# Optimization experiments

Measured on AMD Instinct MI355X. Metric: run time of the kernel, lower is better.

The kernel has to match this reference:

```python
import jax, jax.numpy as jnp
import numpy as np


def _conv(x, w):
    # NCHW 'same' conv, stride 1 (kernel 7 -> pad 3 each side)
    return jax.lax.conv_general_dilated(
        x, w, window_strides=(1, 1), padding='SAME',
        dimension_numbers=('NCHW', 'OIHW', 'NCHW'))


def _run_dir(x, w_ih, w_hh, b, reverse):
    # x: (B, T, C, H, W); returns (B, T, hid, H, W)
    B, T, C, H, W = x.shape
    hid = w_hh.shape[1]
    # Precompute input-to-gate convs for all timesteps at once (fold T into batch)
    xg = _conv(x.reshape(B * T, C, H, W), w_ih) + b[None, :, None, None]
    xg = xg.reshape(B, T, 4 * hid, H, W).transpose(1, 0, 2, 3, 4)  # (T,B,4hid,H,W)
    h0 = jnp.zeros((B, hid, H, W), x.dtype)
    c0 = jnp.zeros_like(h0)

    def step(carry, g_x):
        h, c = carry
        g = g_x + _conv(h, w_hh)
        i, f, gg, o = jnp.split(g, 4, axis=1)  # PyTorch LSTM gate order
        c = jax.nn.sigmoid(f) * c + jax.nn.sigmoid(i) * jnp.tanh(gg)
        h = jax.nn.sigmoid(o) * jnp.tanh(c)
        return (h, c), h

    _, hs = jax.lax.scan(step, (h0, c0), xg, reverse=reverse)
    return hs.transpose(1, 0, 2, 3, 4)  # (B,T,hid,H,W)


def setup_inputs() -> dict:
    key = jax.random.key(0)
    ks = jax.random.split(key, 6)
    B, T, C, H, W = 8, 16, 3, 32, 32
    hid, K = 64, 7
    s_ih = 1.0 / np.sqrt(C * K * K)
    s_hh = 1.0 / np.sqrt(hid * K * K)
    return {
        'x': jax.random.normal(ks[0], (B, T, C, H, W), jnp.float32),
        'w_ih_f': jax.random.normal(ks[1], (4 * hid, C, K, K), jnp.float32) * s_ih,
        'w_hh_f': jax.random.normal(ks[2], (4 * hid, hid, K, K), jnp.float32) * s_hh,
        'b_f': jnp.zeros((4 * hid,), jnp.float32),
        'w_ih_b': jax.random.normal(ks[3], (4 * hid, C, K, K), jnp.float32) * s_ih,
        'w_hh_b': jax.random.normal(ks[4], (4 * hid, hid, K, K), jnp.float32) * s_hh,
        'b_b': jnp.zeros((4 * hid,), jnp.float32),
    }


def reference(x, w_ih_f, w_hh_f, b_f, w_ih_b, w_hh_b, b_b):
    out_f = _run_dir(x, w_ih_f, w_hh_f, b_f, reverse=False)
    out_b = _run_dir(x, w_ih_b, w_hh_b, b_b, reverse=True)
    # bidirectional concat along channel dim -> (B, T, 2*hid, H, W)
    return jnp.concatenate([out_f, out_b], axis=2)
```

## Files before the change

kernel.cpp:

```cpp
#include <hip/hip_runtime.h>
#include <hip/hip_bf16.h>


#define HP0_B  0
#define HP1_B  3112960
#define C_B    6225920
#define WALL_B 10420224
#define BIAS_B 13860864
#define FLAG_B 13862912

using short8 = __attribute__((ext_vector_type(8))) short;
using f32x4  = __attribute__((ext_vector_type(4))) float;

__device__ __forceinline__ float sigm(float x) { return 1.0f / (1.0f + __expf(-x)); }
__device__ __forceinline__ float tanh_f(float x) {
    x = fminf(fmaxf(x, -30.0f), 30.0f);
    float e = __expf(2.0f * x);
    return (e - 1.0f) / (e + 1.0f);
}

__global__ void detect_dtype(const unsigned int* __restrict__ xw, int* __restrict__ flag) {
    int lane = threadIdx.x;
    int cnt = 0;
    for (int i = 0; i < 4; ++i) {
        unsigned int w = xw[lane * 4 + i];
        unsigned int e = (w >> 7) & 0xFFu;
        cnt += (e >= 0xC0u) ? 1 : 0;
    }
#pragma unroll
    for (int off = 32; off > 0; off >>= 1) cnt += __shfl_down(cnt, off, 64);
    if (lane == 0) *flag = (cnt > 16) ? 1 : 0;
}

__global__ void prep_weights(const void* __restrict__ whhf, const void* __restrict__ whhb,
                             const void* __restrict__ wihf, const void* __restrict__ wihb,
                             const void* __restrict__ bf, const void* __restrict__ bb,
                             short* __restrict__ wall, float* __restrict__ bias_r,
                             const int* __restrict__ flag) {
    int n = blockIdx.x * blockDim.x + threadIdx.x;
    const int fp32 = *flag;
    if (n < 1720320) {
        int icl = n & 31;
        int oc = (n >> 5) & 255;
        int ks = (n >> 13) % 105;
        int d = n / 860160;
        const void* hh = d ? whhb : whhf;
        const void* ih = d ? wihb : wihf;
        float v = 0.0f;
        if (ks < 98) {
            int ky = ks / 14, rr = ks % 14, kc = rr / 7, kx = rr % 7;
            int si = ((oc * 64 + kc * 32 + icl) * 7 + ky) * 7 + kx;
            v = fp32 ? ((const float*)hh)[si] : __bfloat162float(((const __hip_bfloat16*)hh)[si]);
        } else {
            int kx = ks - 98, ky = icl >> 2, ic = icl & 3;
            if (ic < 3 && ky < 7) {
                int si = ((oc * 3 + ic) * 7 + ky) * 7 + kx;
                v = fp32 ? ((const float*)ih)[si] : __bfloat162float(((const __hip_bfloat16*)ih)[si]);
            }
        }
        __hip_bfloat16 hv = __float2bfloat16(v);
        wall[n] = *(short*)&hv;
        return;
    }
    n -= 1720320;
    if (n < 512) {
        const void* src = (n >= 256) ? bb : bf;
        int j = n & 255;
        bias_r[n] = fp32 ? ((const float*)src)[j] : __bfloat162float(((const __hip_bfloat16*)src)[j]);
    }
}

__global__ void zero_state(float* __restrict__ ws_f) {
    int n = blockIdx.x * blockDim.x + threadIdx.x;
    if (n < 2605056) ws_f[n] = 0.0f;
}

__global__ __launch_bounds__(512, 2)
void lstm_step(const void* __restrict__ xin,
               const short* __restrict__ wall,
               const float* __restrict__ bias_r,
               const unsigned short* __restrict__ hp_r,
               unsigned short* __restrict__ hp_w,
               float* __restrict__ c,
               void* __restrict__ out,
               const int* __restrict__ flag, int s) {
    const int ygrp = blockIdx.x;
    const int b = blockIdx.y;
    const int dir = blockIdx.z;
    const int t = dir ? (15 - s) : s;
    const int y0 = ygrp * 2;
    const int tid = threadIdx.x;
    const int wv = tid >> 6;
    const int kg = wv >> 2;
    const int wm = wv & 3;
    const int l = tid & 63;
    const int q = l >> 4;
    const int li = l & 15;
    const int fp32 = *flag;
    const int db = dir * 8 + b;

    __shared__ __align__(16) short lds[26240];

    {
        const uint4* src = (const uint4*)(hp_r + (size_t)(db * 38 + y0) * 40 * 64);
        for (int i = tid; i < 2560; i += 512) {
            int ic8 = i & 7, col = (i >> 3) % 40, row = i / 320;
            uint4 v = src[i];
            *(uint4*)&lds[(row * 40 + col) * 72 + ic8 * 8] = v;
        }
    }
    for (int i = tid; i < 3200; i += 512) {
        int k = i % 40, cc = (i / 40) % 40, r = i / 1600;
        float v = 0.0f;
        if (k < 28) {
            int ky = k >> 2, ic = k & 3;
            int yin = y0 + r + ky - 3, cin = cc - 3;
            if (ic < 3 && yin >= 0 && yin < 32 && cin >= 0 && cin < 32) {
                size_t gi = (size_t)((b * 16 + t) * 3 + ic) * 1024 + yin * 32 + cin;
                v = fp32 ? ((const float*)xin)[gi]
                         : __bfloat162float(((const __hip_bfloat16*)xin)[gi]);
            }
        }
        __hip_bfloat16 hb = __float2bfloat16(v);
        lds[23040 + i] = *(short*)&hb;
    }
    __syncthreads();

    f32x4 acc[4][4];
    if (kg == 0) {
        const float* bp = bias_r + dir * 256 + wm * 16 + q * 4;
#pragma unroll
        for (int g = 0; g < 4; ++g) {
            f32x4 bv = *(const f32x4*)(bp + g * 64);
#pragma unroll
            for (int nt = 0; nt < 4; ++nt) acc[g][nt] = bv;
        }
    } else {
        f32x4 z = {0.0f, 0.0f, 0.0f, 0.0f};
#pragma unroll
        for (int g = 0; g < 4; ++g)
#pragma unroll
            for (int nt = 0; nt < 4; ++nt) acc[g][nt] = z;
    }

    const short* wbase = wall + (size_t)dir * 860160 + ((wm * 16 + li) * 32 + q * 8);
    int bh[4], bx[4];
#pragma unroll
    for (int nt = 0; nt < 4; ++nt) {
        int rt = nt >> 1, ct = nt & 1;
        bh[nt] = (rt * 40 + ct * 16 + li) * 72 + q * 8;
        bx[nt] = 23040 + (rt * 40 + ct * 16 + li) * 40 + q * 8;
    }

    auto loadA = [&](short8* A, int ks) {
        const short* p = wbase + (size_t)ks * 8192;
#pragma unroll
        for (int g = 0; g < 4; ++g) A[g] = *(const short8*)(p + g * 2048);
    };
    auto loadB = [&](short8* B, int ks) {
        if (ks < 98) {
            int ky = ks / 14, rr = ks % 14;
            int uoff = ky * 2880 + (rr % 7) * 72 + (rr / 7) * 32;
#pragma unroll
            for (int nt = 0; nt < 4; ++nt) B[nt] = *(const short8*)&lds[bh[nt] + uoff];
        } else {
            int uoff = (ks - 98) * 40;
#pragma unroll
            for (int nt = 0; nt < 4; ++nt) B[nt] = *(const short8*)&lds[bx[nt] + uoff];
        }
    };
    auto mfma16 = [&](short8* A, short8* B) {
#pragma unroll
        for (int g = 0; g < 4; ++g)
#pragma unroll
            for (int nt = 0; nt < 4; ++nt)
                acc[g][nt] = __builtin_amdgcn_mfma_f32_16x16x32_bf16(A[g], B[nt], acc[g][nt], 0, 0, 0);
    };

    const int ks_begin = kg ? 52 : 0;
    const int ks_end   = kg ? 105 : 52;
    short8 A0[4], A1[4], B0[4], B1[4];
    loadA(A0, ks_begin); loadB(B0, ks_begin);
    int ks = ks_begin;
#pragma unroll 1
    for (; ks + 1 < ks_end; ks += 2) {
        loadA(A1, ks + 1); loadB(B1, ks + 1);
        mfma16(A0, B0);
        int kn = (ks + 2 < ks_end) ? ks + 2 : ks;
        loadA(A0, kn); loadB(B0, kn);
        mfma16(A1, B1);
    }
    if (ks < ks_end) mfma16(A0, B0);

    __syncthreads();
    {
        float* exch = (float*)lds;
        float* xp = exch + wm * 2048 + q * 64 + li * 4;
        if (kg == 1) {
#pragma unroll
            for (int g = 0; g < 2; ++g)
#pragma unroll
                for (int nt = 0; nt < 4; ++nt)
                    *(f32x4*)(xp + (g * 4 + nt) * 256) = acc[g][nt];
        }
        __syncthreads();
        if (kg == 0) {
#pragma unroll
            for (int g = 0; g < 2; ++g)
#pragma unroll
                for (int nt = 0; nt < 4; ++nt)
                    acc[g][nt] += *(const f32x4*)(xp + (g * 4 + nt) * 256);
        }
        __syncthreads();
        if (kg == 1) {
#pragma unroll
            for (int g = 0; g < 2; ++g)
#pragma unroll
                for (int nt = 0; nt < 4; ++nt)
                    *(f32x4*)(xp + (g * 4 + nt) * 256) = acc[2 + g][nt];
        }
        __syncthreads();
        if (kg == 0) {
#pragma unroll
            for (int g = 0; g < 2; ++g)
#pragma unroll
                for (int nt = 0; nt < 4; ++nt)
                    acc[2 + g][nt] += *(const f32x4*)(xp + (g * 4 + nt) * 256);
        }
    }
    if (kg == 1) return;

    const int hid0 = wm * 16 + q * 4;
#pragma unroll
    for (int nt = 0; nt < 4; ++nt) {
        int y = y0 + (nt >> 1);
        int px = (nt & 1) * 16 + li;
        float* cp = c + (size_t)(db * 1024 + y * 32 + px) * 64 + hid0;
        f32x4 cold = *(const f32x4*)cp;
        f32x4 hv;
#pragma unroll
        for (int r = 0; r < 4; ++r) {
            float iv = sigm(acc[0][nt][r]);
            float fv = sigm(acc[1][nt][r]);
            float gv = tanh_f(acc[2][nt][r]);
            float ov = sigm(acc[3][nt][r]);
            float cn = fv * cold[r] + iv * gv;
            cold[r] = cn;
            hv[r] = ov * tanh_f(cn);
        }
        *(f32x4*)cp = cold;

        ushort4 hu;
        {
            __hip_bfloat16 t0 = __float2bfloat16(hv[0]); hu.x = *(unsigned short*)&t0;
            __hip_bfloat16 t1 = __float2bfloat16(hv[1]); hu.y = *(unsigned short*)&t1;
            __hip_bfloat16 t2 = __float2bfloat16(hv[2]); hu.z = *(unsigned short*)&t2;
            __hip_bfloat16 t3 = __float2bfloat16(hv[3]); hu.w = *(unsigned short*)&t3;
        }
        *(ushort4*)(hp_w + (size_t)((db * 38 + y + 3) * 40 + px + 3) * 64 + hid0) = hu;

        size_t ob = (size_t)((b * 16 + t) * 128 + dir * 64 + hid0) * 1024 + y * 32 + px;
        if (fp32) {
            float* op = (float*)out;
#pragma unroll
            for (int r = 0; r < 4; ++r) op[ob + (size_t)r * 1024] = hv[r];
        } else {
            __hip_bfloat16* op = (__hip_bfloat16*)out;
#pragma unroll
            for (int r = 0; r < 4; ++r) op[ob + (size_t)r * 1024] = __float2bfloat16(hv[r]);
        }
    }
}

extern "C" void kernel_launch(void* const* d_in, const int* in_sizes, int n_in,
                              void* d_out, int out_size, void* d_ws, size_t ws_size,
                              hipStream_t stream) {
    char* wsb = (char*)d_ws;
    unsigned short* hp0 = (unsigned short*)(wsb + HP0_B);
    unsigned short* hp1 = (unsigned short*)(wsb + HP1_B);
    float* c = (float*)(wsb + C_B);
    short* wall = (short*)(wsb + WALL_B);
    float* bias_r = (float*)(wsb + BIAS_B);
    int* flag = (int*)(wsb + FLAG_B);

    detect_dtype<<<1, 64, 0, stream>>>((const unsigned int*)d_in[0], flag);
    prep_weights<<<6722, 256, 0, stream>>>(d_in[2], d_in[5], d_in[1], d_in[4],
                                           d_in[3], d_in[6], wall, bias_r, flag);
    zero_state<<<10176, 256, 0, stream>>>((float*)d_ws);

    for (int s = 0; s < 16; ++s) {
        unsigned short* hr = (s & 1) ? hp1 : hp0;
        unsigned short* hw = (s & 1) ? hp0 : hp1;
        lstm_step<<<dim3(16, 8, 2), 512, 0, stream>>>(d_in[0], wall, bias_r,
                                                      hr, hw, c, d_out, flag, s);
    }
}
```

Before: 645.8 us.

## Fuse timestep launches into persistent kernel with per-sequence global barriers

Replaces the 16 per-timestep kernel launches with a single persistent kernel of 256 blocks that loops over timesteps internally. The 16 blocks working on each (direction, batch) sequence synchronize through an atomic-counter spin barrier in global memory between steps, so launch overhead and the device-wide launch boundary go away. MFMA sections also get raised wave priority via s_setprio. The design relies on all 256 blocks being co-resident (2 blocks/CU), and the spin barrier has a guard timeout that could silently break ordering if it fires.

```diff
diff --git a/kernel.cpp b/kernel.cpp
--- a/kernel.cpp
+++ b/kernel.cpp
@@ -8,6 +8,7 @@
 #define WALL_B 10420224
 #define BIAS_B 13860864
 #define FLAG_B 13862912
+#define CNT_B  13862916
 
 using short8 = __attribute__((ext_vector_type(8))) short;
 using f32x4  = __attribute__((ext_vector_type(4))) float;
@@ -75,19 +76,34 @@
     if (n < 2605056) ws_f[n] = 0.0f;
 }
 
+__device__ __forceinline__ void db_barrier(int* cnt, int target) {
+    if (threadIdx.x == 0) {
+        __threadfence();
+        __hip_atomic_fetch_add(cnt, 1, __ATOMIC_RELEASE, __HIP_MEMORY_SCOPE_AGENT);
+        int guard = 0;
+        while (__hip_atomic_load(cnt, __ATOMIC_ACQUIRE, __HIP_MEMORY_SCOPE_AGENT) < target) {
+            __builtin_amdgcn_s_sleep(2);
+            if (++guard > (1 << 24)) break;
+        }
+        __threadfence();
+    }
+    __syncthreads();
+}
+
 __global__ __launch_bounds__(512, 2)
-void lstm_step(const void* __restrict__ xin,
-               const short* __restrict__ wall,
-               const float* __restrict__ bias_r,
-               const unsigned short* __restrict__ hp_r,
-               unsigned short* __restrict__ hp_w,
-               float* __restrict__ c,
-               void* __restrict__ out,
-               const int* __restrict__ flag, int s) {
-    const int ygrp = blockIdx.x;
-    const int b = blockIdx.y;
-    const int dir = blockIdx.z;
-    const int t = dir ? (15 - s) : s;
+void lstm_run(const void* __restrict__ xin,
+              const short* __restrict__ wall,
+              const float* __restrict__ bias_r,
+              unsigned short* __restrict__ hp0,
+              unsigned short* __restrict__ hp1,
+              float* __restrict__ c,
+              void* __restrict__ out,
+              const int* __restrict__ flag,
+              int s0, int s1, int* __restrict__ cnt) {
+    const int bid = blockIdx.x;
+    const int dir = bid & 1;
+    const int b = (bid >> 1) & 7;
+    const int ygrp = bid >> 4;
     const int y0 = ygrp * 2;
     const int tid = threadIdx.x;
     const int wv = tid >> 6;
@@ -101,48 +117,6 @@
 
     __shared__ __align__(16) short lds[26240];
 
-    {
-        const uint4* src = (const uint4*)(hp_r + (size_t)(db * 38 + y0) * 40 * 64);
-        for (int i = tid; i < 2560; i += 512) {
-            int ic8 = i & 7, col = (i >> 3) % 40, row = i / 320;
-            uint4 v = src[i];
-            *(uint4*)&lds[(row * 40 + col) * 72 + ic8 * 8] = v;
-        }
-    }
-    for (int i = tid; i < 3200; i += 512) {
-        int k = i % 40, cc = (i / 40) % 40, r = i / 1600;
-        float v = 0.0f;
-        if (k < 28) {
-            int ky = k >> 2, ic = k & 3;
-            int yin = y0 + r + ky - 3, cin = cc - 3;
-            if (ic < 3 && yin >= 0 && yin < 32 && cin >= 0 && cin < 32) {
-                size_t gi = (size_t)((b * 16 + t) * 3 + ic) * 1024 + yin * 32 + cin;
-                v = fp32 ? ((const float*)xin)[gi]
-                         : __bfloat162float(((const __hip_bfloat16*)xin)[gi]);
-            }
-        }
-        __hip_bfloat16 hb = __float2bfloat16(v);
-        lds[23040 + i] = *(short*)&hb;
-    }
-    __syncthreads();
-
-    f32x4 acc[4][4];
-    if (kg == 0) {
-        const float* bp = bias_r + dir * 256 + wm * 16 + q * 4;
-#pragma unroll
-        for (int g = 0; g < 4; ++g) {
-            f32x4 bv = *(const f32x4*)(bp + g * 64);
-#pragma unroll
-            for (int nt = 0; nt < 4; ++nt) acc[g][nt] = bv;
-        }
-    } else {
-        f32x4 z = {0.0f, 0.0f, 0.0f, 0.0f};
-#pragma unroll
-        for (int g = 0; g < 4; ++g)
-#pragma unroll
-            for (int nt = 0; nt < 4; ++nt) acc[g][nt] = z;
-    }
-
     const short* wbase = wall + (size_t)dir * 860160 + ((wm * 16 + li) * 32 + q * 8);
     int bh[4], bx[4];
 #pragma unroll
@@ -151,124 +125,179 @@
         bh[nt] = (rt * 40 + ct * 16 + li) * 72 + q * 8;
         bx[nt] = 23040 + (rt * 40 + ct * 16 + li) * 40 + q * 8;
     }
-
-    auto loadA = [&](short8* A, int ks) {
-        const short* p = wbase + (size_t)ks * 8192;
-#pragma unroll
-        for (int g = 0; g < 4; ++g) A[g] = *(const short8*)(p + g * 2048);
-    };
-    auto loadB = [&](short8* B, int ks) {
-        if (ks < 98) {
-            int ky = ks / 14, rr = ks % 14;
-            int uoff = ky * 2880 + (rr % 7) * 72 + (rr / 7) * 32;
-#pragma unroll
-            for (int nt = 0; nt < 4; ++nt) B[nt] = *(const short8*)&lds[bh[nt] + uoff];
-        } else {
-            int uoff = (ks - 98) * 40;
-#pragma unroll
-            for (int nt = 0; nt < 4; ++nt) B[nt] = *(const short8*)&lds[bx[nt] + uoff];
-        }
-    };
-    auto mfma16 = [&](short8* A, short8* B) {
-#pragma unroll
-        for (int g = 0; g < 4; ++g)
-#pragma unroll
-            for (int nt = 0; nt < 4; ++nt)
-                acc[g][nt] = __builtin_amdgcn_mfma_f32_16x16x32_bf16(A[g], B[nt], acc[g][nt], 0, 0, 0);
-    };
-
     const int ks_begin = kg ? 52 : 0;
     const int ks_end   = kg ? 105 : 52;
-    short8 A0[4], A1[4], B0[4], B1[4];
-    loadA(A0, ks_begin); loadB(B0, ks_begin);
-    int ks = ks_begin;
+
 #pragma unroll 1
-    for (; ks + 1 < ks_end; ks += 2) {
-        loadA(A1, ks + 1); loadB(B1, ks + 1);
-        mfma16(A0, B0);
-        int kn = (ks + 2 < ks_end) ? ks + 2 : ks;
-        loadA(A0, kn); loadB(B0, kn);
-        mfma16(A1, B1);
-    }
-    if (ks < ks_end) mfma16(A0, B0);
-
-    __syncthreads();
-    {
-        float* exch = (float*)lds;
-        float* xp = exch + wm * 2048 + q * 64 + li * 4;
-        if (kg == 1) {
-#pragma unroll
-            for (int g = 0; g < 2; ++g)
+    for (int s = s0; s < s1; ++s) {
+        const int t = dir ? (15 - s) : s;
+        const unsigned short* hp_r = (s & 1) ? hp1 : hp0;
+        unsigned short* hp_w = (s & 1) ? hp0 : hp1;
+
+        {
+            const uint4* src = (const uint4*)(hp_r + (size_t)(db * 38 + y0) * 40 * 64);
+            for (int i = tid; i < 2560; i += 512) {
+                int ic8 = i & 7, col = (i >> 3) % 40, row = i / 320;
+                uint4 v = src[i];
+                *(uint4*)&lds[(row * 40 + col) * 72 + ic8 * 8] = v;
+            }
+        }
+        for (int i = tid; i < 3200; i += 512) {
+            int k = i % 40, cc = (i / 40) % 40, r = i / 1600;
+            float v = 0.0f;
+            if (k < 28) {
+                int ky = k >> 2, ic = k & 3;
+                int yin = y0 + r + ky - 3, cin = cc - 3;
+                if (ic < 3 && yin >= 0 && yin < 32 && cin >= 0 && cin < 32) {
+                    size_t gi = (size_t)((b * 16 + t) * 3 + ic) * 1024 + yin * 32 + cin;
+                    v = fp32 ? ((const float*)xin)[gi]
+                             : __bfloat162float(((const __hip_bfloat16*)xin)[gi]);
+                }
+            }
+            __hip_bfloat16 hb = __float2bfloat16(v);
+            lds[23040 + i] = *(short*)&hb;
+        }
+        __syncthreads();
+
+        f32x4 acc[4][4];
+        if (kg == 0) {
+            const float* bp = bias_r + dir * 256 + wm * 16 + q * 4;
+#pragma unroll
+            for (int g = 0; g < 4; ++g) {
+                f32x4 bv = *(const f32x4*)(bp + g * 64);
+#pragma unroll
+                for (int nt = 0; nt < 4; ++nt) acc[g][nt] = bv;
+            }
+        } else {
+            f32x4 z = {0.0f, 0.0f, 0.0f, 0.0f};
+#pragma unroll
+            for (int g = 0; g < 4; ++g)
+#pragma unroll
+                for (int nt = 0; nt < 4; ++nt) acc[g][nt] = z;
+        }
+
+        auto loadA = [&](short8* A, int ks) {
+            const short* p = wbase + (size_t)ks * 8192;
+#pragma unroll
+            for (int g = 0; g < 4; ++g) A[g] = *(const short8*)(p + g * 2048);
+        };
+        auto loadB = [&](short8* B, int ks) {
+            if (ks < 98) {
+                int ky = ks / 14, rr = ks % 14;
+                int uoff = ky * 2880 + (rr % 7) * 72 + (rr / 7) * 32;
+#pragma unroll
+                for (int nt = 0; nt < 4; ++nt) B[nt] = *(const short8*)&lds[bh[nt] + uoff];
+            } else {
+                int uoff = (ks - 98) * 40;
+#pragma unroll
+                for (int nt = 0; nt < 4; ++nt) B[nt] = *(const short8*)&lds[bx[nt] + uoff];
+            }
+        };
+        auto mfma16 = [&](short8* A, short8* B) {
+            __builtin_amdgcn_s_setprio(1);
+#pragma unroll
+            for (int g = 0; g < 4; ++g)
 #pragma unroll
                 for (int nt = 0; nt < 4; ++nt)
-                    *(f32x4*)(xp + (g * 4 + nt) * 256) = acc[g][nt];
-        }
+                    acc[g][nt] = __builtin_amdgcn_mfma_f32_16x16x32_bf16(A[g], B[nt], acc[g][nt], 0, 0, 0);
+            __builtin_amdgcn_s_setprio(0);
+        };
+
+        short8 A0[4], A1[4], B0[4], B1[4];
+        loadA(A0, ks_begin); loadB(B0, ks_begin);
+        int ks = ks_begin;
+#pragma unroll 1
+        for (; ks + 1 < ks_end; ks += 2) {
+            loadA(A1, ks + 1); loadB(B1, ks + 1);
+            mfma16(A0, B0);
+            int kn = (ks + 2 < ks_end) ? ks + 2 : ks;
+            loadA(A0, kn); loadB(B0, kn);
+            mfma16(A1, B1);
+        }
+        if (ks < ks_end) mfma16(A0, B0);
+
         __syncthreads();
+        {
+            float* exch = (float*)lds;
+            float* xp = exch + wm * 2048 + q * 64 + li * 4;
+            if (kg == 1) {
+#pragma unroll
+                for (int g = 0; g < 2; ++g)
+#pragma unroll
+                    for (int nt = 0; nt < 4; ++nt)
+                        *(f32x4*)(xp + (g * 4 + nt) * 256) = acc[g][nt];
+            }
+            __syncthreads();
+            if (kg == 0) {
+#pragma unroll
+                for (int g = 0; g < 2; ++g)
+#pragma unroll
+                    for (int nt = 0; nt < 4; ++nt)
+                        acc[g][nt] += *(const f32x4*)(xp + (g * 4 + nt) * 256);
+            }
+            __syncthreads();
+            if (kg == 1) {
+#pragma unroll
+                for (int g = 0; g < 2; ++g)
+#pragma unroll
+                    for (int nt = 0; nt < 4; ++nt)
+                        *(f32x4*)(xp + (g * 4 + nt) * 256) = acc[2 + g][nt];
+            }
+            __syncthreads();
+            if (kg == 0) {
+#pragma unroll
+                for (int g = 0; g < 2; ++g)
+#pragma unroll
+                    for (int nt = 0; nt < 4; ++nt)
+                        acc[2 + g][nt] += *(const f32x4*)(xp + (g * 4 + nt) * 256);
+            }
+        }
+
         if (kg == 0) {
-#pragma unroll
-            for (int g = 0; g < 2; ++g)
-#pragma unroll
-                for (int nt = 0; nt < 4; ++nt)
-                    acc[g][nt] += *(const f32x4*)(xp + (g * 4 + nt) * 256);
-        }
+            const int hid0 = wm * 16 + q * 4;
+#pragma unroll
+            for (int nt = 0; nt < 4; ++nt) {
+                int y = y0 + (nt >> 1);
+                int px = (nt & 1) * 16 + li;
+                float* cp = c + (size_t)(db * 1024 + y * 32 + px) * 64 + hid0;
+                f32x4 cold = *(const f32x4*)cp;
+                f32x4 hv;
+#pragma unroll
+                for (int r = 0; r < 4; ++r) {
+                    float iv = sigm(acc[0][nt][r]);
+                    float fv = sigm(acc[1][nt][r]);
+                    float gv = tanh_f(acc[2][nt][r]);
+                    float ov = sigm(acc[3][nt][r]);
+                    float cn = fv * cold[r] + iv * gv;
+                    cold[r] = cn;
+                    hv[r] = ov * tanh_f(cn);
+                }
+                *(f32x4*)cp = cold;
+
+                ushort4 hu;
+                {
+                    __hip_bfloat16 t0 = __float2bfloat16(hv[0]); hu.x = *(unsigned short*)&t0;
+                    __hip_bfloat16 t1 = __float2bfloat16(hv[1]); hu.y = *(unsigned short*)&t1;
+                    __hip_bfloat16 t2 = __float2bfloat16(hv[2]); hu.z = *(unsigned short*)&t2;
+                    __hip_bfloat16 t3 = __float2bfloat16(hv[3]); hu.w = *(unsigned short*)&t3;
+                }
+                *(ushort4*)(hp_w + (size_t)((db * 38 + y + 3) * 40 + px + 3) * 64 + hid0) = hu;
+
+                size_t ob = (size_t)((b * 16 + t) * 128 + dir * 64 + hid0) * 1024 + y * 32 + px;
+                if (fp32) {
+                    float* op = (float*)out;
+#pragma unroll
+                    for (int r = 0; r < 4; ++r) op[ob + (size_t)r * 1024] = hv[r];
+                } else {
+                    __hip_bfloat16* op = (__hip_bfloat16*)out;
+#pragma unroll
+                    for (int r = 0; r < 4; ++r) op[ob + (size_t)r * 1024] = __float2bfloat16(hv[r]);
+                }
+            }
+        }
+
         __syncthreads();
-        if (kg == 1) {
-#pragma unroll
-            for (int g = 0; g < 2; ++g)
-#pragma unroll
-                for (int nt = 0; nt < 4; ++nt)
-                    *(f32x4*)(xp + (g * 4 + nt) * 256) = acc[2 + g][nt];
-        }
-        __syncthreads();
-        if (kg == 0) {
-#pragma unroll
-            for (int g = 0; g < 2; ++g)
-#pragma unroll
-                for (int nt = 0; nt < 4; ++nt)
-                    acc[2 + g][nt] += *(const f32x4*)(xp + (g * 4 + nt) * 256);
-        }
-    }
-    if (kg == 1) return;
-
-    const int hid0 = wm * 16 + q * 4;
-#pragma unroll
-    for (int nt = 0; nt < 4; ++nt) {
-        int y = y0 + (nt >> 1);
-        int px = (nt & 1) * 16 + li;
-        float* cp = c + (size_t)(db * 1024 + y * 32 + px) * 64 + hid0;
-        f32x4 cold = *(const f32x4*)cp;
-        f32x4 hv;
-#pragma unroll
-        for (int r = 0; r < 4; ++r) {
-            float iv = sigm(acc[0][nt][r]);
-            float fv = sigm(acc[1][nt][r]);
-            float gv = tanh_f(acc[2][nt][r]);
-            float ov = sigm(acc[3][nt][r]);
-            float cn = fv * cold[r] + iv * gv;
-            cold[r] = cn;
-            hv[r] = ov * tanh_f(cn);
-        }
-        *(f32x4*)cp = cold;
-
-        ushort4 hu;
-        {
-            __hip_bfloat16 t0 = __float2bfloat16(hv[0]); hu.x = *(unsigned short*)&t0;
-            __hip_bfloat16 t1 = __float2bfloat16(hv[1]); hu.y = *(unsigned short*)&t1;
-            __hip_bfloat16 t2 = __float2bfloat16(hv[2]); hu.z = *(unsigned short*)&t2;
-            __hip_bfloat16 t3 = __float2bfloat16(hv[3]); hu.w = *(unsigned short*)&t3;
-        }
-        *(ushort4*)(hp_w + (size_t)((db * 38 + y + 3) * 40 + px + 3) * 64 + hid0) = hu;
-
-        size_t ob = (size_t)((b * 16 + t) * 128 + dir * 64 + hid0) * 1024 + y * 32 + px;
-        if (fp32) {
-            float* op = (float*)out;
-#pragma unroll
-            for (int r = 0; r < 4; ++r) op[ob + (size_t)r * 1024] = hv[r];
-        } else {
-            __hip_bfloat16* op = (__hip_bfloat16*)out;
-#pragma unroll
-            for (int r = 0; r < 4; ++r) op[ob + (size_t)r * 1024] = __float2bfloat16(hv[r]);
-        }
+        if (s + 1 < s1) db_barrier(&cnt[db], 16 * (s + 1));
     }
 }
 
@@ -282,16 +311,23 @@
     short* wall = (short*)(wsb + WALL_B);
     float* bias_r = (float*)(wsb + BIAS_B);
     int* flag = (int*)(wsb + FLAG_B);
+    int* cnt = (int*)(wsb + CNT_B);
 
     detect_dtype<<<1, 64, 0, stream>>>((const unsigned int*)d_in[0], flag);
     prep_weights<<<6722, 256, 0, stream>>>(d_in[2], d_in[5], d_in[1], d_in[4],
                                            d_in[3], d_in[6], wall, bias_r, flag);
     zero_state<<<10176, 256, 0, stream>>>((float*)d_ws);
 
-    for (int s = 0; s < 16; ++s) {
-        unsigned short* hr = (s & 1) ? hp1 : hp0;
-        unsigned short* hw = (s & 1) ? hp0 : hp1;
-        lstm_step<<<dim3(16, 8, 2), 512, 0, stream>>>(d_in[0], wall, bias_r,
-                                                      hr, hw, c, d_out, flag, s);
-    }
-}
+    const bool persist = (ws_size >= (size_t)(CNT_B + 64));
+    if (persist) {
+        hipMemsetAsync(cnt, 0, 64, stream);
+        lstm_run<<<dim3(256), 512, 0, stream>>>(d_in[0], wall, bias_r,
+                                                hp0, hp1, c, d_out, flag,
+                                                0, 16, cnt);
+    } else {
+        for (int s = 0; s < 16; ++s)
+            lstm_run<<<dim3(256), 512, 0, stream>>>(d_in[0], wall, bias_r,
+                                                    hp0, hp1, c, d_out, flag,
+                                                    s, s + 1, nullptr);
+    }
+}
```

Measured after the change: 935.9 us. +44.9%, slower.

## Stage weights into LDS via async global_load_lds pipeline with 4-wave blocks

Applied to the files above, without the earlier changes.

Rewrites the per-step LSTM kernel to use 256-thread blocks that cover the full K range each, instead of splitting K across two wave groups. Weight tiles are streamed into a 4-deep LDS ring buffer using asynchronous global_load_lds with vmcnt waits, so global weight fetches overlap the MFMA work. It also raises wave priority around the MFMA bursts and flattens the grid to 1D. The kernel needs about 118 KB of dynamic LDS and runs one block per CU, which lowers occupancy. A fallback kernel is used if the large LDS attribute cannot be set.

```diff
diff --git a/kernel.cpp b/kernel.cpp
--- a/kernel.cpp
+++ b/kernel.cpp
@@ -8,6 +8,9 @@
 #define WALL_B 10420224
 #define BIAS_B 13860864
 #define FLAG_B 13862912
+
+#define AOFF   26240
+#define LDS_BYTES 118016
 
 using short8 = __attribute__((ext_vector_type(8))) short;
 using f32x4  = __attribute__((ext_vector_type(4))) float;
@@ -75,7 +78,9 @@
     if (n < 2605056) ws_f[n] = 0.0f;
 }
 
-__global__ __launch_bounds__(512, 2)
+#define WAITV(n) asm volatile("s_waitcnt vmcnt(" #n ")" ::: "memory")
+
+__global__ __launch_bounds__(256, 1)
 void lstm_step(const void* __restrict__ xin,
                const short* __restrict__ wall,
                const float* __restrict__ bias_r,
@@ -84,9 +89,187 @@
                float* __restrict__ c,
                void* __restrict__ out,
                const int* __restrict__ flag, int s) {
-    const int ygrp = blockIdx.x;
-    const int b = blockIdx.y;
-    const int dir = blockIdx.z;
+    extern __shared__ short lds[];
+    const int bid = blockIdx.x;
+    const int dir = bid & 1;
+    const int b = (bid >> 1) & 7;
+    const int ygrp = bid >> 4;
+    const int t = dir ? (15 - s) : s;
+    const int y0 = ygrp * 2;
+    const int tid = threadIdx.x;
+    const int wv = tid >> 6;
+    const int l = tid & 63;
+    const int q = l >> 4;
+    const int li = l & 15;
+    const int fp32 = *flag;
+    const int db = dir * 8 + b;
+
+    const short* wdir = wall + (size_t)dir * 860160;
+
+    const int glane = (wv * 16 + li) * 32 + q * 8;
+    const int lwave = AOFF + wv * 2048;
+
+    auto stageA = [&](int ks) {
+        const short* gp = wdir + (size_t)ks * 8192 + glane;
+        short* lp = &lds[lwave + ((ks & 3) << 13)];
+#pragma unroll
+        for (int g = 0; g < 4; ++g) {
+            __builtin_amdgcn_global_load_lds(
+                (const __attribute__((address_space(1))) int*)(gp + g * 2048),
+                (__attribute__((address_space(3))) int*)(lp + g * 512),
+                16, 0, 0);
+        }
+    };
+
+    stageA(0); stageA(1); stageA(2);
+
+    {
+        const uint4* src = (const uint4*)(hp_r + (size_t)(db * 38 + y0) * 40 * 64);
+        for (int i = tid; i < 2560; i += 256) {
+            int ic8 = i & 7, col = (i >> 3) % 40, row = i / 320;
+            uint4 v = src[i];
+            *(uint4*)&lds[(row * 40 + col) * 72 + ic8 * 8] = v;
+        }
+    }
+    for (int i = tid; i < 3200; i += 256) {
+        int k = i % 40, cc = (i / 40) % 40, r = i / 1600;
+        float v = 0.0f;
+        if (k < 28) {
+            int ky = k >> 2, ic = k & 3;
+            int yin = y0 + r + ky - 3, cin = cc - 3;
+            if (ic < 3 && yin >= 0 && yin < 32 && cin >= 0 && cin < 32) {
+                size_t gi = (size_t)((b * 16 + t) * 3 + ic) * 1024 + yin * 32 + cin;
+                v = fp32 ? ((const float*)xin)[gi]
+                         : __bfloat162float(((const __hip_bfloat16*)xin)[gi]);
+            }
+        }
+        __hip_bfloat16 hb = __float2bfloat16(v);
+        lds[23040 + i] = *(short*)&hb;
+    }
+    __syncthreads();
+
+    f32x4 acc[4][4];
+    {
+        const float* bp = bias_r + dir * 256 + wv * 16 + q * 4;
+#pragma unroll
+        for (int g = 0; g < 4; ++g) {
+            f32x4 bv = *(const f32x4*)(bp + g * 64);
+#pragma unroll
+            for (int nt = 0; nt < 4; ++nt) acc[g][nt] = bv;
+        }
+    }
+
+    int bh[4], bx[4];
+#pragma unroll
+    for (int nt = 0; nt < 4; ++nt) {
+        int rt = nt >> 1, ct = nt & 1;
+        bh[nt] = (rt * 40 + ct * 16 + li) * 72 + q * 8;
+        bx[nt] = 23040 + (rt * 40 + ct * 16 + li) * 40 + q * 8;
+    }
+
+    auto loadA = [&](short8* A, int ks) {
+        const short* p = &lds[lwave + ((ks & 3) << 13) + l * 8];
+#pragma unroll
+        for (int g = 0; g < 4; ++g) A[g] = *(const short8*)(p + g * 512);
+    };
+    auto loadB = [&](short8* B, int ks) {
+        if (ks < 98) {
+            int ky = ks / 14, rr = ks % 14;
+            int uoff = ky * 2880 + (rr % 7) * 72 + (rr / 7) * 32;
+#pragma unroll
+            for (int nt = 0; nt < 4; ++nt) B[nt] = *(const short8*)&lds[bh[nt] + uoff];
+        } else {
+            int uoff = (ks - 98) * 40;
+#pragma unroll
+            for (int nt = 0; nt < 4; ++nt) B[nt] = *(const short8*)&lds[bx[nt] + uoff];
+        }
+    };
+    auto mfma16 = [&](short8* A, short8* B) {
+        __builtin_amdgcn_s_setprio(1);
+#pragma unroll
+        for (int g = 0; g < 4; ++g)
+#pragma unroll
+            for (int nt = 0; nt < 4; ++nt)
+                acc[g][nt] = __builtin_amdgcn_mfma_f32_16x16x32_bf16(A[g], B[nt], acc[g][nt], 0, 0, 0);
+        __builtin_amdgcn_s_setprio(0);
+    };
+
+    short8 Aa[4], Ba[4], Ab[4], Bb[4];
+    loadA(Aa, 0); loadB(Ba, 0);
+#pragma unroll 1
+    for (int ks = 0; ks < 102; ks += 2) {
+        stageA(ks + 3);
+        WAITV(8);
+        loadA(Ab, ks + 1); loadB(Bb, ks + 1);
+        mfma16(Aa, Ba);
+        stageA(ks + 4);
+        WAITV(8);
+        loadA(Aa, ks + 2); loadB(Ba, ks + 2);
+        mfma16(Ab, Bb);
+    }
+    WAITV(4);
+    loadA(Ab, 103); loadB(Bb, 103);
+    mfma16(Aa, Ba);
+    WAITV(0);
+    loadA(Aa, 104); loadB(Ba, 104);
+    mfma16(Ab, Bb);
+    mfma16(Aa, Ba);
+
+    const int hid0 = wv * 16 + q * 4;
+#pragma unroll
+    for (int nt = 0; nt < 4; ++nt) {
+        int y = y0 + (nt >> 1);
+        int px = (nt & 1) * 16 + li;
+        float* cp = c + (size_t)(db * 1024 + y * 32 + px) * 64 + hid0;
+        f32x4 cold = *(const f32x4*)cp;
+        f32x4 hv;
+#pragma unroll
+        for (int r = 0; r < 4; ++r) {
+            float iv = sigm(acc[0][nt][r]);
+            float fv = sigm(acc[1][nt][r]);
+            float gv = tanh_f(acc[2][nt][r]);
+            float ov = sigm(acc[3][nt][r]);
+            float cn = fv * cold[r] + iv * gv;
+            cold[r] = cn;
+            hv[r] = ov * tanh_f(cn);
+        }
+        *(f32x4*)cp = cold;
+
+        ushort4 hu;
+        {
+            __hip_bfloat16 t0 = __float2bfloat16(hv[0]); hu.x = *(unsigned short*)&t0;
+            __hip_bfloat16 t1 = __float2bfloat16(hv[1]); hu.y = *(unsigned short*)&t1;
+            __hip_bfloat16 t2 = __float2bfloat16(hv[2]); hu.z = *(unsigned short*)&t2;
+            __hip_bfloat16 t3 = __float2bfloat16(hv[3]); hu.w = *(unsigned short*)&t3;
+        }
+        *(ushort4*)(hp_w + (size_t)((db * 38 + y + 3) * 40 + px + 3) * 64 + hid0) = hu;
+
+        size_t ob = (size_t)((b * 16 + t) * 128 + dir * 64 + hid0) * 1024 + y * 32 + px;
+        if (fp32) {
+            float* op = (float*)out;
+#pragma unroll
+            for (int r = 0; r < 4; ++r) op[ob + (size_t)r * 1024] = hv[r];
+        } else {
+            __hip_bfloat16* op = (__hip_bfloat16*)out;
+#pragma unroll
+            for (int r = 0; r < 4; ++r) op[ob + (size_t)r * 1024] = __float2bfloat16(hv[r]);
+        }
+    }
+}
+
+__global__ __launch_bounds__(512, 2)
+void lstm_step_fb(const void* __restrict__ xin,
+                  const short* __restrict__ wall,
+                  const float* __restrict__ bias_r,
+                  const unsigned short* __restrict__ hp_r,
+                  unsigned short* __restrict__ hp_w,
+                  float* __restrict__ c,
+                  void* __restrict__ out,
+                  const int* __restrict__ flag, int s) {
+    const int bid = blockIdx.x;
+    const int dir = bid & 1;
+    const int b = (bid >> 1) & 7;
+    const int ygrp = bid >> 4;
     const int t = dir ? (15 - s) : s;
     const int y0 = ygrp * 2;
     const int tid = threadIdx.x;
@@ -170,11 +353,13 @@
         }
     };
     auto mfma16 = [&](short8* A, short8* B) {
+        __builtin_amdgcn_s_setprio(1);
 #pragma unroll
         for (int g = 0; g < 4; ++g)
 #pragma unroll
             for (int nt = 0; nt < 4; ++nt)
                 acc[g][nt] = __builtin_amdgcn_mfma_f32_16x16x32_bf16(A[g], B[nt], acc[g][nt], 0, 0, 0);
+        __builtin_amdgcn_s_setprio(0);
     };
 
     const int ks_begin = kg ? 52 : 0;
@@ -283,15 +468,32 @@
     float* bias_r = (float*)(wsb + BIAS_B);
     int* flag = (int*)(wsb + FLAG_B);
 
+    static int big_lds_ok = -1;
+    if (big_lds_ok < 0) {
+        hipError_t e = hipFuncSetAttribute((const void*)lstm_step,
+                                           hipFuncAttributeMaxDynamicSharedMemorySize,
+                                           LDS_BYTES);
+        big_lds_ok = (e == hipSuccess) ? 1 : 0;
+    }
+
     detect_dtype<<<1, 64, 0, stream>>>((const unsigned int*)d_in[0], flag);
     prep_weights<<<6722, 256, 0, stream>>>(d_in[2], d_in[5], d_in[1], d_in[4],
                                            d_in[3], d_in[6], wall, bias_r, flag);
     zero_state<<<10176, 256, 0, stream>>>((float*)d_ws);
 
-    for (int s = 0; s < 16; ++s) {
-        unsigned short* hr = (s & 1) ? hp1 : hp0;
-        unsigned short* hw = (s & 1) ? hp0 : hp1;
-        lstm_step<<<dim3(16, 8, 2), 512, 0, stream>>>(d_in[0], wall, bias_r,
-                                                      hr, hw, c, d_out, flag, s);
-    }
-}
+    if (big_lds_ok) {
+        for (int s = 0; s < 16; ++s) {
+            unsigned short* hr = (s & 1) ? hp1 : hp0;
+            unsigned short* hw = (s & 1) ? hp0 : hp1;
+            lstm_step<<<dim3(256), 256, LDS_BYTES, stream>>>(d_in[0], wall, bias_r,
+                                                             hr, hw, c, d_out, flag, s);
+        }
+    } else {
+        for (int s = 0; s < 16; ++s) {
+            unsigned short* hr = (s & 1) ? hp1 : hp0;
+            unsigned short* hw = (s & 1) ? hp0 : hp1;
+            lstm_step_fb<<<dim3(256), 512, 0, stream>>>(d_in[0], wall, bias_r,
+                                                        hr, hw, c, d_out, flag, s);
+        }
+    }
+}
```

Result: slower. 725.9 us (+12.4%).
